# Kernel tuning notes

Hardware: AMD Instinct MI355X
Metric: run time of the kernel (lower is better)

Reference implementation:

```python
import jax, jax.numpy as jnp
import numpy as np

N_WIRES = 12
N_LAYERS = 3
DIM = 2 ** N_WIRES
BATCH = 512


def _rot_matrix(a, b, c):
    """Fused U = RZ(c) @ RY(b) @ RX(a) as a 2x2 complex64 matrix."""
    ca, sa = jnp.cos(a * 0.5), jnp.sin(a * 0.5)
    cb, sb = jnp.cos(b * 0.5), jnp.sin(b * 0.5)
    ec = jnp.exp(-0.5j * c)  # e^{-i c/2}
    zero = jnp.zeros_like(ec)
    RX = jnp.stack([jnp.stack([ca + 0j, -1j * sa]),
                    jnp.stack([-1j * sa, ca + 0j])]).astype(jnp.complex64)
    RY = jnp.stack([jnp.stack([cb, -sb]),
                    jnp.stack([sb, cb])]).astype(jnp.complex64)
    RZ = jnp.stack([jnp.stack([ec, zero]),
                    jnp.stack([zero, jnp.conj(ec)])]).astype(jnp.complex64)
    return RZ @ RY @ RX


def _apply_1q(psi, U, wire):
    B = psi.shape[0]
    dl, dr = 2 ** wire, 2 ** (N_WIRES - wire - 1)
    s = psi.reshape(B, dl, 2, dr)
    s = jnp.einsum('ij,bljr->blir', U, s)
    return s.reshape(B, DIM)


def _apply_cnot_adjacent(psi, wire):
    # CNOT(control=wire, target=wire+1): permute (10 <-> 11) on the joint axis
    B = psi.shape[0]
    dl, dr = 2 ** wire, 2 ** (N_WIRES - wire - 2)
    s = psi.reshape(B, dl, 4, dr)
    s = jnp.take(s, jnp.array([0, 1, 3, 2]), axis=2)
    return s.reshape(B, DIM)


def _circuit(state_batch, weights):
    psi = state_batch.astype(jnp.complex64)  # QubitStateVector init
    for l in range(N_LAYERS):
        for w in range(N_WIRES):
            U = _rot_matrix(weights[l, w, 0], weights[l, w, 1], weights[l, w, 2])
            psi = _apply_1q(psi, U, w)
        for w in range(N_WIRES - 1):  # 'cnot' chain entanglement
            psi = _apply_cnot_adjacent(psi, w)
    B = state_batch.shape[0]
    probs = (psi.real ** 2 + psi.imag ** 2).reshape((B,) + (2,) * N_WIRES)
    feats = []
    for w in range(N_WIRES):  # <Z_w> = p(0) - p(1)
        axes = tuple(a for a in range(1, N_WIRES + 1) if a != w + 1)
        p = probs.sum(axis=axes)  # (B, 2)
        feats.append(p[:, 0] - p[:, 1])
    return jnp.stack(feats, axis=-1)  # (B, N_WIRES)


def setup_inputs() -> dict:
    key = jax.random.key(0)
    k1, k2, k3, k4 = jax.random.split(key, 4)
    state = jax.random.normal(k1, (BATCH, DIM), dtype=jnp.float32)
    state = state / jnp.linalg.norm(state, axis=-1, keepdims=True)  # valid quantum states
    weights = jax.random.uniform(k2, (N_LAYERS, N_WIRES, 3), dtype=jnp.float32,
                                 minval=0.0, maxval=2.0 * np.pi)
    head_w = jax.random.normal(k3, (1, N_WIRES), dtype=jnp.float32) / np.sqrt(N_WIRES)
    head_b = jax.random.normal(k4, (1,), dtype=jnp.float32) * 0.01
    return {"state_batch": state, "weights": weights, "head_w": head_w, "head_b": head_b}


def reference(state_batch, weights, head_w, head_b):
    feats = _circuit(state_batch, weights)          # (B, N_WIRES) PauliZ expvals
    out = feats @ head_w.T + head_b                 # Linear(num_wires, 1)
    return out[:, 0]                                # squeeze(-1) -> (B,)
```

## Files before the change

kernel.cpp:

```cpp
#include <hip/hip_runtime.h>


namespace {

typedef float v2f __attribute__((ext_vector_type(2)));

constexpr int N_WIRES  = 12;
constexpr int DIM      = 1 << N_WIRES;
constexpr int THREADS  = 256;
constexpr int PER      = 16;
constexpr int NGATES   = 36;
constexpr int PADC     = 4606;

__device__ __forceinline__ v2f cmul(v2f u, v2f p) {
    v2f d;
    asm("v_pk_mul_f32 %0, %1, %2 op_sel_hi:[1,0]"
        : "=v"(d) : "v"(p), "v"(u));
    asm("v_pk_fma_f32 %0, %1, %2, %0 op_sel:[1,1,0] op_sel_hi:[0,1,1] neg_lo:[0,1,0]"
        : "+v"(d) : "v"(p), "v"(u));
    return d;
}
__device__ __forceinline__ void cfma(v2f& d, v2f u, v2f p) {
    asm("v_pk_fma_f32 %0, %1, %2, %0 op_sel_hi:[1,0,1]"
        : "+v"(d) : "v"(p), "v"(u));
    asm("v_pk_fma_f32 %0, %1, %2, %0 op_sel:[1,1,0] op_sel_hi:[0,1,1] neg_lo:[0,1,0]"
        : "+v"(d) : "v"(p), "v"(u));
}

__device__ __forceinline__ void apply4(v2f amp[PER], const v2f (*Um)[4], int gbase)
{
    #pragma unroll
    for (int gg = 0; gg < 4; ++gg) {
        const v2f u00 = Um[gbase + gg][0];
        const v2f u01 = Um[gbase + gg][1];
        const v2f u10 = Um[gbase + gg][2];
        const v2f u11 = Um[gbase + gg][3];
        const int st = 8 >> gg;
        #pragma unroll
        for (int k0 = 0; k0 < PER; ++k0) {
            if (k0 & st) continue;
            const int k1 = k0 | st;
            const v2f p = amp[k0], q = amp[k1];
            v2f np = cmul(u00, p); cfma(np, u01, q);
            v2f nq = cmul(u10, p); cfma(nq, u11, q);
            amp[k0] = np;
            amp[k1] = nq;
        }
    }
}

__global__ __launch_bounds__(THREADS, 4)
void qcirc_kernel(const float* __restrict__ state,
                  const float* __restrict__ weights,
                  const float* __restrict__ head_w,
                  const float* __restrict__ head_b,
                  float* __restrict__ out)
{
    __shared__ __align__(16) v2f buf[PADC];
    __shared__ __align__(16) v2f Umat[NGATES][4];
    __shared__ float redbuf[THREADS / 64];

    const int t = threadIdx.x;
    const int b = blockIdx.x;

    if (t < NGATES) {
        const float* wp = weights + t * 3;
        float ha = 0.5f * wp[0], hb = 0.5f * wp[1], hc = 0.5f * wp[2];
        float ca = cosf(ha), sa = sinf(ha);
        float cb = cosf(hb), sb = sinf(hb);
        float ecr = cosf(hc), eci = -sinf(hc);
        float t0 = cb * ca, t1 = sb * sa, t2 = sb * ca, t3 = cb * sa;
        float u00r =  ecr * t0 - eci * t1;
        float u00i =  ecr * t1 + eci * t0;
        float u10r =  ecr * t2 - eci * t3;
        float u10i = -ecr * t3 - eci * t2;
        Umat[t][0] = (v2f){ u00r,  u00i};
        Umat[t][1] = (v2f){-u10r,  u10i};
        Umat[t][2] = (v2f){ u10r,  u10i};
        Umat[t][3] = (v2f){ u00r, -u00i};
    }

    const int T  = t >> 4, u = t & 15;
    const int bA = 18 * T + u;
    const int bB = 288 * T + u;
    const int bC = 18 * t;
    const int tb  = t ^ (t >> 1);
    const int tbx = tb ^ 128;
    const int pb0 = 18 * (tb  >> 4) + (tb  & 15);
    const int pb1 = 18 * (tbx >> 4) + (tbx & 15);

    float hw[N_WIRES];
    #pragma unroll
    for (int w = 0; w < N_WIRES; ++w) hw[w] = head_w[w];
    int it = t ^ (t >> 1); it ^= it >> 2; it ^= it >> 4;
    float chi = 0.f;
    #pragma unroll
    for (int w = 0; w < 8; ++w)
        chi += ((it >> (7 - w)) & 1) ? -hw[w] : hw[w];
    const int parfill = (__popc(t) & 1) ? 0xF : 0;

    v2f amp[PER];
    {
        const float* sp = state + (size_t)b * DIM;
        #pragma unroll
        for (int k = 0; k < PER; ++k)
            amp[k] = (v2f){sp[(k << 8) | t], 0.f};
    }
    __syncthreads();

    #pragma unroll
    for (int l = 0; l < 3; ++l) {
        const int gb = l * 12;
        if (l > 0) {
            #pragma unroll
            for (int k = 0; k < PER; ++k) {
                const int g = k ^ (k >> 1);
                amp[k] = buf[((k & 1) ? pb1 : pb0) + 288 * g];
            }
            __syncthreads();
        }

        apply4(amp, Umat, gb + 0);
        #pragma unroll
        for (int k = 0; k < PER; ++k) buf[bA + 288 * k] = amp[k];
        __syncthreads();

        #pragma unroll
        for (int k = 0; k < PER; ++k) amp[k] = buf[bB + 18 * k];
        apply4(amp, Umat, gb + 4);
        #pragma unroll
        for (int k = 0; k < PER; ++k) buf[bB + 18 * k] = amp[k];
        __syncthreads();

        {
            const float4* r = reinterpret_cast<const float4*>(&buf[bC]);
            #pragma unroll
            for (int k = 0; k < PER / 2; ++k) {
                float4 v = r[k];
                amp[2 * k]     = (v2f){v.x, v.y};
                amp[2 * k + 1] = (v2f){v.z, v.w};
            }
        }
        apply4(amp, Umat, gb + 8);
        if (l < 2) {
            float4* w = reinterpret_cast<float4*>(&buf[bC]);
            #pragma unroll
            for (int k = 0; k < PER / 2; ++k)
                w[k] = make_float4(amp[2 * k].x, amp[2 * k].y,
                                   amp[2 * k + 1].x, amp[2 * k + 1].y);
            __syncthreads();
        }
    }

    float acc = 0.f;
    #pragma unroll
    for (int k = 0; k < PER; ++k) {
        int ml = (k ^ (k >> 1)); ml ^= ml >> 2; ml ^= parfill;
        float c = chi;
        c += ((ml >> 3) & 1) ? -hw[8]  : hw[8];
        c += ((ml >> 2) & 1) ? -hw[9]  : hw[9];
        c += ((ml >> 1) & 1) ? -hw[10] : hw[10];
        c += ( ml       & 1) ? -hw[11] : hw[11];
        float p = amp[k].x * amp[k].x + amp[k].y * amp[k].y;
        acc += p * c;
    }

    #pragma unroll
    for (int off = 32; off > 0; off >>= 1)
        acc += __shfl_down(acc, off, 64);
    if ((t & 63) == 0) redbuf[t >> 6] = acc;
    __syncthreads();
    if (t == 0) {
        float s = 0.f;
        #pragma unroll
        for (int q = 0; q < THREADS / 64; ++q) s += redbuf[q];
        out[b] = s + head_b[0];
    }
}

}

extern "C" void kernel_launch(void* const* d_in, const int* in_sizes, int n_in,
                              void* d_out, int out_size, void* d_ws, size_t ws_size,
                              hipStream_t stream)
{
    const float* state   = (const float*)d_in[0];
    const float* weights = (const float*)d_in[1];
    const float* head_w  = (const float*)d_in[2];
    const float* head_b  = (const float*)d_in[3];
    float* out = (float*)d_out;

    const int batch = in_sizes[0] / DIM;
    qcirc_kernel<<<batch, THREADS, 0, stream>>>(state, weights, head_w, head_b, out);
}
```

Measured before the change: 76.59 us.

## Use 512 threads with wavefront shuffle gates instead of LDS transposes

Doubles threads per block and halves the amplitudes each thread holds. Six of the twelve single-qubit gates per layer now exchange amplitudes between lanes with ds_swizzle and shfl_xor rather than going through shared memory. This cuts LDS round-trips and barriers per layer and gives more parallelism per batch element. The state load becomes vectorized float4, and the CNOT permutation and parity bookkeeping are re-derived for the new index mapping. In exchange, shuffles cost extra instructions and register traffic, and the gate order changed, so correctness depends on the new index algebra being right.

```diff
diff --git a/kernel.cpp b/kernel.cpp
--- a/kernel.cpp
+++ b/kernel.cpp
@@ -7,8 +7,8 @@
 
 constexpr int N_WIRES  = 12;
 constexpr int DIM      = 1 << N_WIRES;
-constexpr int THREADS  = 256;
-constexpr int PER      = 16;
+constexpr int THREADS  = 512;
+constexpr int PER      = 8;
 constexpr int NGATES   = 36;
 constexpr int PADC     = 4606;
 
@@ -27,15 +27,15 @@
         : "+v"(d) : "v"(p), "v"(u));
 }
 
-__device__ __forceinline__ void apply4(v2f amp[PER], const v2f (*Um)[4], int gbase)
-{
-    #pragma unroll
-    for (int gg = 0; gg < 4; ++gg) {
+__device__ __forceinline__ void apply3(v2f amp[PER], const v2f (*Um)[4], int gbase)
+{
+    #pragma unroll
+    for (int gg = 0; gg < 3; ++gg) {
         const v2f u00 = Um[gbase + gg][0];
         const v2f u01 = Um[gbase + gg][1];
         const v2f u10 = Um[gbase + gg][2];
         const v2f u11 = Um[gbase + gg][3];
-        const int st = 8 >> gg;
+        const int st = 4 >> gg;
         #pragma unroll
         for (int k0 = 0; k0 < PER; ++k0) {
             if (k0 & st) continue;
@@ -46,6 +46,38 @@
             amp[k0] = np;
             amp[k1] = nq;
         }
+    }
+}
+
+template<int MASK>
+__device__ __forceinline__ float shx(float v) {
+    if constexpr (MASK == 32) {
+        return __shfl_xor(v, 32, 64);
+    } else {
+        return __int_as_float(__builtin_amdgcn_ds_swizzle(
+            __float_as_int(v), (MASK << 10) | 0x1F));
+    }
+}
+
+template<int MASK>
+__device__ __forceinline__ void shuffle_gate(v2f amp[PER], const v2f (*Um)[4],
+                                             int g, int t)
+{
+    const v2f u00 = Um[g][0], u01 = Um[g][1], u10 = Um[g][2], u11 = Um[g][3];
+    const bool hi = (t & MASK) != 0;
+    const v2f ua = hi ? u11 : u00;
+    const v2f ub = hi ? u10 : u01;
+    v2f q[PER];
+    #pragma unroll
+    for (int k = 0; k < PER; ++k) {
+        q[k].x = shx<MASK>(amp[k].x);
+        q[k].y = shx<MASK>(amp[k].y);
+    }
+    #pragma unroll
+    for (int k = 0; k < PER; ++k) {
+        v2f n = cmul(ua, amp[k]);
+        cfma(n, ub, q[k]);
+        amp[k] = n;
     }
 }
 
@@ -80,87 +112,80 @@
         Umat[t][3] = (v2f){ u00r, -u00i};
     }
 
-    const int T  = t >> 4, u = t & 15;
-    const int bA = 18 * T + u;
-    const int bB = 288 * T + u;
-    const int bC = 18 * t;
-    const int tb  = t ^ (t >> 1);
-    const int tbx = tb ^ 128;
-    const int pb0 = 18 * (tb  >> 4) + (tb  & 15);
-    const int pb1 = 18 * (tbx >> 4) + (tbx & 15);
-
-    float hw[N_WIRES];
-    #pragma unroll
-    for (int w = 0; w < N_WIRES; ++w) hw[w] = head_w[w];
-    int it = t ^ (t >> 1); it ^= it >> 2; it ^= it >> 4;
-    float chi = 0.f;
-    #pragma unroll
-    for (int w = 0; w < 8; ++w)
-        chi += ((it >> (7 - w)) & 1) ? -hw[w] : hw[w];
-    const int parfill = (__popc(t) & 1) ? 0xF : 0;
+    const int bD = 18 * (t >> 1) + ((t & 1) << 3);
+    const int bT = 18 * (t >> 4) + (t & 15);
+    const int gb    = t ^ (t >> 1);
+    const int gbase = 18 * (gb >> 1) + ((gb & 1) << 3);
+    const int tx4   = (t & 1) << 2;
 
     v2f amp[PER];
     {
-        const float* sp = state + (size_t)b * DIM;
+        const float4* sp = reinterpret_cast<const float4*>(
+            state + (size_t)b * DIM + (t << 3));
+        float4 a0 = sp[0], a1 = sp[1];
+        amp[0] = (v2f){a0.x, 0.f}; amp[1] = (v2f){a0.y, 0.f};
+        amp[2] = (v2f){a0.z, 0.f}; amp[3] = (v2f){a0.w, 0.f};
+        amp[4] = (v2f){a1.x, 0.f}; amp[5] = (v2f){a1.y, 0.f};
+        amp[6] = (v2f){a1.z, 0.f}; amp[7] = (v2f){a1.w, 0.f};
+    }
+    __syncthreads();
+
+    #pragma unroll
+    for (int l = 0; l < 3; ++l) {
+        const int g0 = l * 12;
+        if (l > 0) {
+            const v2f* gp = &buf[gbase + tx4];
+            const v2f* gm = &buf[gbase - tx4];
+            amp[0] = gp[0]; amp[1] = gp[1]; amp[2] = gp[3]; amp[3] = gp[2];
+            amp[4] = gm[6]; amp[5] = gm[7]; amp[6] = gm[5]; amp[7] = gm[4];
+        }
+
+        apply3(amp, Umat, g0 + 9);
+        shuffle_gate<32>(amp, Umat, g0 + 3, t);
+        shuffle_gate<16>(amp, Umat, g0 + 4, t);
+        shuffle_gate< 8>(amp, Umat, g0 + 5, t);
+        shuffle_gate< 4>(amp, Umat, g0 + 6, t);
+        shuffle_gate< 2>(amp, Umat, g0 + 7, t);
+        shuffle_gate< 1>(amp, Umat, g0 + 8, t);
+
+        if (l > 0) __syncthreads();
+        {
+            float4* w = reinterpret_cast<float4*>(&buf[bD]);
+            w[0] = make_float4(amp[0].x, amp[0].y, amp[1].x, amp[1].y);
+            w[1] = make_float4(amp[2].x, amp[2].y, amp[3].x, amp[3].y);
+            w[2] = make_float4(amp[4].x, amp[4].y, amp[5].x, amp[5].y);
+            w[3] = make_float4(amp[6].x, amp[6].y, amp[7].x, amp[7].y);
+        }
+        __syncthreads();
+
         #pragma unroll
-        for (int k = 0; k < PER; ++k)
-            amp[k] = (v2f){sp[(k << 8) | t], 0.f};
-    }
-    __syncthreads();
-
-    #pragma unroll
-    for (int l = 0; l < 3; ++l) {
-        const int gb = l * 12;
-        if (l > 0) {
+        for (int k = 0; k < PER; ++k) amp[k] = buf[bT + 576 * k];
+        apply3(amp, Umat, g0 + 0);
+        if (l < 2) {
             #pragma unroll
-            for (int k = 0; k < PER; ++k) {
-                const int g = k ^ (k >> 1);
-                amp[k] = buf[((k & 1) ? pb1 : pb0) + 288 * g];
-            }
+            for (int k = 0; k < PER; ++k) buf[bT + 576 * k] = amp[k];
             __syncthreads();
         }
-
-        apply4(amp, Umat, gb + 0);
-        #pragma unroll
-        for (int k = 0; k < PER; ++k) buf[bA + 288 * k] = amp[k];
-        __syncthreads();
-
-        #pragma unroll
-        for (int k = 0; k < PER; ++k) amp[k] = buf[bB + 18 * k];
-        apply4(amp, Umat, gb + 4);
-        #pragma unroll
-        for (int k = 0; k < PER; ++k) buf[bB + 18 * k] = amp[k];
-        __syncthreads();
-
-        {
-            const float4* r = reinterpret_cast<const float4*>(&buf[bC]);
-            #pragma unroll
-            for (int k = 0; k < PER / 2; ++k) {
-                float4 v = r[k];
-                amp[2 * k]     = (v2f){v.x, v.y};
-                amp[2 * k + 1] = (v2f){v.z, v.w};
-            }
-        }
-        apply4(amp, Umat, gb + 8);
-        if (l < 2) {
-            float4* w = reinterpret_cast<float4*>(&buf[bC]);
-            #pragma unroll
-            for (int k = 0; k < PER / 2; ++k)
-                w[k] = make_float4(amp[2 * k].x, amp[2 * k].y,
-                                   amp[2 * k + 1].x, amp[2 * k + 1].y);
-            __syncthreads();
-        }
-    }
+    }
+
+    float hw[N_WIRES];
+    #pragma unroll
+    for (int w = 0; w < N_WIRES; ++w) hw[w] = head_w[w];
+    int it = t ^ (t >> 1); it ^= it >> 2; it ^= it >> 4; it ^= it >> 8;
+    float chi = 0.f;
+    #pragma unroll
+    for (int w = 3; w < 12; ++w)
+        chi += ((it >> (11 - w)) & 1) ? -hw[w] : hw[w];
 
     float acc = 0.f;
     #pragma unroll
     for (int k = 0; k < PER; ++k) {
-        int ml = (k ^ (k >> 1)); ml ^= ml >> 2; ml ^= parfill;
-        float c = chi;
-        c += ((ml >> 3) & 1) ? -hw[8]  : hw[8];
-        c += ((ml >> 2) & 1) ? -hw[9]  : hw[9];
-        c += ((ml >> 1) & 1) ? -hw[10] : hw[10];
-        c += ( ml       & 1) ? -hw[11] : hw[11];
+        const int m3 = (k ^ (k >> 1) ^ (k >> 2)) & 7;
+        const int p3 = __popc(k) & 1;
+        float c = p3 ? -chi : chi;
+        c += (m3 & 4) ? -hw[0] : hw[0];
+        c += (m3 & 2) ? -hw[1] : hw[1];
+        c += (m3 & 1) ? -hw[2] : hw[2];
         float p = amp[k].x * amp[k].x + amp[k].y * amp[k].y;
         acc += p * c;
     }
```

Measured after the change: 77.75 us. About the same (+1.5%).
